# Kernel tuning notes

Hardware: AMD Instinct MI355X
Metric: run time of the kernel (lower is better)

Reference implementation:

```python
import jax, jax.numpy as jnp
import numpy as np

N = 1_000_000   # mesh points
D_IN = 5        # scalar invariants
H = 128         # hidden width
L = 5           # hidden layers
NB = 10         # tensor bases

# t0 generator basis rows (flattened 3x3 deviatoric diag tensors)
T01 = np.array([-1/3, 0, 0, 0, 1/6, 0, 0, 0, 1/6], dtype=np.float32)
T02 = np.array([1/6, 0, 0, 0, -1/3, 0, 0, 0, 1/6], dtype=np.float32)
T03 = np.array([1/6, 0, 0, 0, 1/6, 0, 0, 0, -1/3], dtype=np.float32)


def _linear_params(k, fan_in, fan_out):
    # xavier_uniform_ with gain=1.0, bias filled with 0.01 (as in init_w_and_b)
    limit = float(np.sqrt(6.0 / (fan_in + fan_out)))
    W = jax.random.uniform(k, (fan_in, fan_out), jnp.float32, -limit, limit)
    b = jnp.full((fan_out,), 0.01, jnp.float32)
    return W, b


def setup_inputs() -> dict:
    key = jax.random.key(0)
    ks = jax.random.split(key, 16)
    x = jax.random.normal(ks[0], (N, D_IN), jnp.float32)
    tb = jax.random.normal(ks[1], (N, NB, 9), jnp.float32)
    inp = {"x": x, "tb": tb}
    dims = [D_IN] + [H] * L
    for i in range(L):
        W, b = _linear_params(ks[2 + i], dims[i], dims[i + 1])
        inp[f"W{i+1}"] = W
        inp[f"b{i+1}"] = b
    inp["Wc"], inp["bc"] = _linear_params(ks[2 + L], H, NB)
    inp["Wg1"], inp["bg1"] = _linear_params(ks[3 + L], H, 1)
    inp["Wg2"], inp["bg2"] = _linear_params(ks[4 + L], H, 1)
    inp["Wg3"], inp["bg3"] = _linear_params(ks[5 + L], H, 1)
    return inp


def reference(x, tb, W1, b1, W2, b2, W3, b3, W4, b4, W5, b5,
              Wc, bc, Wg1, bg1, Wg2, bg2, Wg3, bg3):
    h = x
    for W, b in ((W1, b1), (W2, b2), (W3, b3), (W4, b4), (W5, b5)):
        h = jax.nn.relu(h @ W + b)          # [N, H]
    coeffs = h @ Wc + bc                     # [N, NB]
    g1 = h @ Wg1 + bg1                       # [N, 1]
    g2 = h @ Wg2 + bg2
    g3 = h @ Wg3 + bg3
    t0 = g1 * jnp.asarray(T01) + g2 * jnp.asarray(T02) + g3 * jnp.asarray(T03)  # [N, 9]
    # batched tensor-basis contraction replacing the per-point double loop
    bij = t0 + jnp.einsum('nt,ntc->nc', coeffs, tb)  # [N, 9]
    return bij
```

## Files before the change

kernel.cpp:

```cpp
#include <hip/hip_runtime.h>
#include <stdint.h>


#define NPTS   1000000
#define TPB    256
#define NBLKS  512
#define PTILE  128
#define NT     ((NPTS + PTILE - 1) / PTILE)

typedef uint32_t u32;
typedef __attribute__((ext_vector_type(4)))  u32   u32x4;
typedef __attribute__((ext_vector_type(8)))  short s16x8;
typedef __attribute__((ext_vector_type(16))) float f32x16;
typedef __attribute__((ext_vector_type(4), aligned(4))) float f32x4u;

#define WS_H(l)   ((l)*32768)
#define WS_Lo(l)  (131072 + (l)*32768)
#define WS_TAIL   262144
#define WS_W1     (WS_TAIL + 8192)
#define WS_BIAS   (WS_TAIL + 12288)

#define LDS_BUFH   0
#define LDS_BUFL   32768
#define LDS_HEADS  65536
#define LDS_W1     (65536 + 8192)
#define LDS_BIAS   (65536 + 12288)
#define LDS_TOTAL  81920

#define MFMA(a,b,c) __builtin_amdgcn_mfma_f32_32x32x16_bf16((a),(b),(c),0,0,0)
#define BC16(v)     __builtin_bit_cast(s16x8, (v))

__device__ __forceinline__ u32 cvtpk(float lo, float hi) {
    u32 r;
    asm("v_cvt_pk_bf16_f32 %0, %1, %2" : "=v"(r) : "v"(lo), "v"(hi));
    return r;
}
__device__ __forceinline__ float lo2f(u32 p){ return __builtin_bit_cast(float, p << 16); }
__device__ __forceinline__ float hi2f(u32 p){ return __builtin_bit_cast(float, p & 0xffff0000u); }
__device__ __forceinline__ uint16_t f2bf(float f) {
    u32 u = __builtin_bit_cast(u32, f);
    return (uint16_t)((u + 0x7fffu + ((u >> 16) & 1u)) >> 16);
}
__device__ __forceinline__ float b2f(uint16_t h){ return __builtin_bit_cast(float, (u32)h << 16); }

__device__ __forceinline__ void stage32(const char* g, char* l, int tid) {
    const int w = tid >> 6, ln = tid & 63;
    const char* gp = g + w*1024 + ln*16;
    char* lp = l + w*1024;
    #pragma unroll
    for (int i = 0; i < 8; ++i)
        __builtin_amdgcn_global_load_lds(
            (const __attribute__((address_space(1))) uint32_t*)(gp + i*4096),
            (__attribute__((address_space(3))) uint32_t*)(lp + i*4096), 16, 0, 0);
}
__device__ __forceinline__ void stage16(const char* g, char* l, int tid) {
    const int w = tid >> 6, ln = tid & 63;
    const char* gp = g + w*1024 + ln*16;
    char* lp = l + w*1024;
    #pragma unroll
    for (int i = 0; i < 4; ++i)
        __builtin_amdgcn_global_load_lds(
            (const __attribute__((address_space(1))) uint32_t*)(gp + i*4096),
            (__attribute__((address_space(3))) uint32_t*)(lp + i*4096), 16, 0, 0);
}

extern "C" __global__ void __launch_bounds__(256)
tbnn_prep(const float* __restrict__ W1, const float* __restrict__ b1,
          const float* __restrict__ W2, const float* __restrict__ b2,
          const float* __restrict__ W3, const float* __restrict__ b3,
          const float* __restrict__ W4, const float* __restrict__ b4,
          const float* __restrict__ W5, const float* __restrict__ b5,
          const float* __restrict__ Wc, const float* __restrict__ bc,
          const float* __restrict__ Wg1,const float* __restrict__ bg1,
          const float* __restrict__ Wg2,const float* __restrict__ bg2,
          const float* __restrict__ Wg3,const float* __restrict__ bg3,
          char* __restrict__ ws)
{
    int idx = blockIdx.x*256 + threadIdx.x;
    if (idx < 65536) {
        int l = idx >> 14, r = idx & 16383, ifc = r >> 7, of = r & 127;
        const float* Wt = (l==0)?W2:(l==1)?W3:(l==2)?W4:W5;
        float w = Wt[ifc*128 + of];
        uint16_t hb = f2bf(w);
        uint16_t lb = f2bf(w - b2f(hb));
        int o = (2*ifc) ^ ((of&7)<<4);
        *(uint16_t*)(ws + WS_H(l)  + of*256 + o) = hb;
        *(uint16_t*)(ws + WS_Lo(l) + of*256 + o) = lb;
    } else if (idx < 65536 + 2048) {
        int j = idx - 65536, of = j >> 7, ifc = j & 127;
        float v = 0.f;
        if      (of < 10)  v = Wc[ifc*10 + of];
        else if (of == 10) v = Wg1[ifc];
        else if (of == 11) v = Wg2[ifc];
        else if (of == 12) v = Wg3[ifc];
        uint16_t hb = f2bf(v);
        uint16_t lb = f2bf(v - b2f(hb));
        char* row = ws + WS_TAIL + of*512;
        int o = (2*ifc) ^ ((of&7)<<4);
        *(uint16_t*)(row + o)       = hb;
        *(uint16_t*)(row + 256 + o) = lb;
    } else if (idx < 65536 + 2048 + 128) {
        int of = idx - (65536 + 2048);
        uint16_t* dst = (uint16_t*)(ws + WS_W1 + of*32);
        #pragma unroll
        for (int s = 0; s < 5; ++s) {
            float w = W1[s*128 + of];
            uint16_t hb = f2bf(w);
            dst[s]      = hb;
            dst[6 + s]  = f2bf(w - b2f(hb));
            dst[11 + s] = hb;
        }
        dst[5] = f2bf(b1[of]);
    } else if (idx < 65536 + 2048 + 128 + 544) {
        int j = idx - (65536 + 2048 + 128);
        float v = 0.f;
        if (j < 512) {
            int l = j >> 7, of = j & 127;
            const float* bt = (l==0)?b2:(l==1)?b3:(l==2)?b4:b5;
            v = bt[of];
        } else {
            int of = j - 512;
            if      (of < 10)  v = bc[of];
            else if (of == 10) v = bg1[0];
            else if (of == 11) v = bg2[0];
            else if (of == 12) v = bg3[0];
        }
        *(uint16_t*)(ws + WS_BIAS + j*2) = f2bf(v);
    }
}

extern "C" __global__ void __launch_bounds__(TPB, 2)
tbnn_main(const float* __restrict__ x, const float* __restrict__ tb,
          const char* __restrict__ ws, float* __restrict__ out)
{
    extern __shared__ char smem[];
    const int tid  = threadIdx.x;
    const int wave = tid >> 6;
    const int lane = tid & 63;
    const int col  = lane & 31;
    const int hi   = lane >> 5;
    const int sm   = (col & 7) << 4;
    const int hib  = hi * 16;

    stage16(ws + WS_TAIL, smem + LDS_HEADS, tid);
    stage32(ws + WS_H(0), smem + LDS_BUFH, tid);
    __syncthreads();

    u32x4 Bc; Bc[0] = hi ? 0u : 0x00003F80u; Bc[1]=0u; Bc[2]=0u; Bc[3]=0u;
    f32x16 zf;
    #pragma unroll
    for (int i = 0; i < 16; ++i) zf[i] = 0.f;

    for (int t = blockIdx.x; t < NT; t += gridDim.x) {
        const int pb = t*PTILE + wave*32;
        const int p  = pb + col;

        f32x16 acc[4];
        u32x4  Bh[8], Bl[8];

        auto convert = [&]() {
            #pragma unroll
            for (int ot = 0; ot < 4; ++ot) {
                f32x16 a = acc[ot];
                #pragma unroll
                for (int h2 = 0; h2 < 2; ++h2) {
                    float e0 = fmaxf(a[8*h2+0], 0.f), e1 = fmaxf(a[8*h2+1], 0.f);
                    float e2 = fmaxf(a[8*h2+2], 0.f), e3 = fmaxf(a[8*h2+3], 0.f);
                    float e4 = fmaxf(a[8*h2+4], 0.f), e5 = fmaxf(a[8*h2+5], 0.f);
                    float e6 = fmaxf(a[8*h2+6], 0.f), e7 = fmaxf(a[8*h2+7], 0.f);
                    u32 h01 = cvtpk(e0,e1), h23 = cvtpk(e2,e3);
                    u32 h45 = cvtpk(e4,e5), h67 = cvtpk(e6,e7);
                    u32 l01 = cvtpk(e0 - lo2f(h01), e1 - hi2f(h01));
                    u32 l23 = cvtpk(e2 - lo2f(h23), e3 - hi2f(h23));
                    u32 l45 = cvtpk(e4 - lo2f(h45), e5 - hi2f(h45));
                    u32 l67 = cvtpk(e6 - lo2f(h67), e7 - hi2f(h67));
                    auto sh1 = __builtin_amdgcn_permlane32_swap(h01, h45, false, false);
                    auto sh2 = __builtin_amdgcn_permlane32_swap(h23, h67, false, false);
                    u32x4 fh; fh[0]=sh1[0]; fh[1]=sh2[0]; fh[2]=sh1[1]; fh[3]=sh2[1];
                    Bh[2*ot+h2] = fh;
                    auto sl1 = __builtin_amdgcn_permlane32_swap(l01, l45, false, false);
                    auto sl2 = __builtin_amdgcn_permlane32_swap(l23, l67, false, false);
                    u32x4 fl; fl[0]=sl1[0]; fl[1]=sl2[0]; fl[2]=sl1[1]; fl[3]=sl2[1];
                    Bl[2*ot+h2] = fl;
                }
            }
        };

        stage32(ws + WS_Lo(0), smem + LDS_BUFL, tid);
        {
            float x0=0.f,x1=0.f,x2=0.f,x3=0.f,x4=0.f;
            if (p < NPTS) {
                const float* xp = x + (size_t)p*5;
                f32x4u v = *(const f32x4u*)xp;
                x0=v.x; x1=v.y; x2=v.z; x3=v.w; x4=xp[4];
            }
            float h0 = lo2f(cvtpk(x0,x0)), l0 = x0 - h0;
            float h1 = lo2f(cvtpk(x1,x1)), l1 = x1 - h1;
            float h2 = lo2f(cvtpk(x2,x2)), l2 = x2 - h2;
            float h3 = lo2f(cvtpk(x3,x3)), l3 = x3 - h3;
            float h4 = lo2f(cvtpk(x4,x4)), l4 = x4 - h4;
            u32x4 Bx;
            if (hi == 0) {
                Bx[0] = cvtpk(h0,h1); Bx[1] = cvtpk(h2,h3);
                Bx[2] = cvtpk(h4,1.0f); Bx[3] = cvtpk(h0,h1);
            } else {
                Bx[0] = cvtpk(h2,h3); Bx[1] = cvtpk(h4,l0);
                Bx[2] = cvtpk(l1,l2); Bx[3] = cvtpk(l3,l4);
            }
            #pragma unroll
            for (int ot = 0; ot < 4; ++ot) {
                u32x4 Av = *(const u32x4*)(smem + LDS_W1 + (ot*32+col)*32 + hib);
                acc[ot] = MFMA(BC16(Av), BC16(Bx), zf);
            }
        }
        convert();
        __syncthreads();

        for (int l = 0; l < 4; ++l) {
            if (l) stage32(ws + WS_Lo(l), smem + LDS_BUFL, tid);
            __builtin_amdgcn_s_setprio(1);
            #pragma unroll
            for (int k = 0; k < 8; ++k) {
                int so = (k*32 + hib) ^ sm;
                const char* rp = smem + LDS_BUFH + col*256 + so;
                u32x4 A0 = *(const u32x4*)(rp);
                u32x4 A1 = *(const u32x4*)(rp + 32*256);
                u32x4 A2 = *(const u32x4*)(rp + 64*256);
                u32x4 A3 = *(const u32x4*)(rp + 96*256);
                s16x8 bl = BC16(Bl[k]), bh = BC16(Bh[k]);
                acc[0] = MFMA(BC16(A0), bl, (k==0)?zf:acc[0]);
                acc[1] = MFMA(BC16(A1), bl, (k==0)?zf:acc[1]);
                acc[2] = MFMA(BC16(A2), bl, (k==0)?zf:acc[2]);
                acc[3] = MFMA(BC16(A3), bl, (k==0)?zf:acc[3]);
                acc[0] = MFMA(BC16(A0), bh, acc[0]);
                acc[1] = MFMA(BC16(A1), bh, acc[1]);
                acc[2] = MFMA(BC16(A2), bh, acc[2]);
                acc[3] = MFMA(BC16(A3), bh, acc[3]);
            }
            __builtin_amdgcn_s_setprio(0);
            __syncthreads();

            stage32(ws + WS_H(l==3 ? 0 : l+1), smem + LDS_BUFH, tid);
            __builtin_amdgcn_s_setprio(1);
            #pragma unroll
            for (int k = 0; k < 8; ++k) {
                int so = (k*32 + hib) ^ sm;
                const char* rp = smem + LDS_BUFL + col*256 + so;
                s16x8 bh = BC16(Bh[k]);
                u32x4 A0 = *(const u32x4*)(rp);
                u32x4 A1 = *(const u32x4*)(rp + 32*256);
                u32x4 A2 = *(const u32x4*)(rp + 64*256);
                u32x4 A3 = *(const u32x4*)(rp + 96*256);
                acc[0] = MFMA(BC16(A0), bh, acc[0]);
                acc[1] = MFMA(BC16(A1), bh, acc[1]);
                acc[2] = MFMA(BC16(A2), bh, acc[2]);
                acc[3] = MFMA(BC16(A3), bh, acc[3]);
            }
            #pragma unroll
            for (int ot = 0; ot < 4; ++ot) {
                u32 bw = (u32)*(const uint16_t*)(smem + LDS_BIAS + (l*128 + ot*32 + col)*2);
                u32x4 Ab; Ab[0] = hi ? 0u : bw; Ab[1]=0u; Ab[2]=0u; Ab[3]=0u;
                acc[ot] = MFMA(BC16(Ab), BC16(Bc), acc[ot]);
            }
            __builtin_amdgcn_s_setprio(0);
            convert();
            __syncthreads();
        }

        f32x16 h6;
        __builtin_amdgcn_s_setprio(1);
        #pragma unroll
        for (int k = 0; k < 8; ++k) {
            int so = (k*32 + hib) ^ sm;
            const char* rp = smem + LDS_HEADS + (col&15)*512;
            u32x4 AvH = *(const u32x4*)(rp + so);
            u32x4 AvL = *(const u32x4*)(rp + 256 + so);
            h6 = MFMA(BC16(AvH), BC16(Bl[k]), (k==0)?zf:h6);
            h6 = MFMA(BC16(AvH), BC16(Bh[k]), h6);
            h6 = MFMA(BC16(AvL), BC16(Bh[k]), h6);
        }
        {
            u32 bw = (u32)*(const uint16_t*)(smem + LDS_BIAS + (512 + col)*2);
            u32x4 Ab; Ab[0] = hi ? 0u : bw; Ab[1]=0u; Ab[2]=0u; Ab[3]=0u;
            h6 = MFMA(BC16(Ab), BC16(Bc), h6);
        }
        __builtin_amdgcn_s_setprio(0);

        if (p < NPTS) {
            const float* tbp = tb + (size_t)p*90;
            f32x16 c = h6;
            const float sixth = 0.16666666666666666f;
            const float third = 0.3333333333333333f;
            float s[9];
            if (hi == 0) {
                float g1 = c[6], g2 = c[7];
                s[0] = -g1*third + g2*sixth;
                s[4] =  g1*sixth - g2*third;
                s[8] =  g1*sixth + g2*sixth;
            } else {
                float g3 = c[4];
                s[0] =  g3*sixth;
                s[4] =  g3*sixth;
                s[8] = -g3*third;
            }
            s[1]=s[2]=s[3]=s[5]=s[6]=s[7]=0.f;
            #pragma unroll
            for (int j = 0; j < 4; ++j) {
                int trow = (hi ? 4 : 0) + j;
                float cf = c[j];
                const float* r = tbp + trow*9;
                f32x4u r0 = *(const f32x4u*)(r);
                f32x4u r1 = *(const f32x4u*)(r + 4);
                float r8 = r[8];
                s[0] += cf*r0.x; s[1] += cf*r0.y; s[2] += cf*r0.z; s[3] += cf*r0.w;
                s[4] += cf*r1.x; s[5] += cf*r1.y; s[6] += cf*r1.z; s[7] += cf*r1.w;
                s[8] += cf*r8;
            }
            if (hi == 0) {
                #pragma unroll
                for (int j = 4; j < 6; ++j) {
                    int trow = 4 + j;
                    float cf = c[j];
                    const float* r = tbp + trow*9;
                    f32x4u r0 = *(const f32x4u*)(r);
                    f32x4u r1 = *(const f32x4u*)(r + 4);
                    float r8 = r[8];
                    s[0] += cf*r0.x; s[1] += cf*r0.y; s[2] += cf*r0.z; s[3] += cf*r0.w;
                    s[4] += cf*r1.x; s[5] += cf*r1.y; s[6] += cf*r1.z; s[7] += cf*r1.w;
                    s[8] += cf*r8;
                }
            }
            #pragma unroll
            for (int j = 0; j < 9; ++j) {
                u32 uv = __builtin_bit_cast(u32, s[j]);
                auto rr = __builtin_amdgcn_permlane32_swap(uv, uv, false, false);
                s[j] = __builtin_bit_cast(float, (u32)rr[0]) + __builtin_bit_cast(float, (u32)rr[1]);
            }
            if (hi == 0) {
                float* op = out + (size_t)p*9;
                f32x4u o0, o1;
                o0.x=s[0]; o0.y=s[1]; o0.z=s[2]; o0.w=s[3];
                o1.x=s[4]; o1.y=s[5]; o1.z=s[6]; o1.w=s[7];
                *(f32x4u*)op       = o0;
                *(f32x4u*)(op + 4) = o1;
                op[8] = s[8];
            }
        }
    }
    __syncthreads();
}

extern "C" void kernel_launch(void* const* d_in, const int* in_sizes, int n_in,
                              void* d_out, int out_size, void* d_ws, size_t ws_size,
                              hipStream_t stream) {
    (void)in_sizes; (void)n_in; (void)out_size; (void)ws_size;
    char* ws = (char*)d_ws;
    hipLaunchKernelGGL(tbnn_prep, dim3(267), dim3(256), 0, stream,
        (const float*)d_in[2],  (const float*)d_in[3],
        (const float*)d_in[4],  (const float*)d_in[5],
        (const float*)d_in[6],  (const float*)d_in[7],
        (const float*)d_in[8],  (const float*)d_in[9],
        (const float*)d_in[10], (const float*)d_in[11],
        (const float*)d_in[12], (const float*)d_in[13],
        (const float*)d_in[14], (const float*)d_in[15],
        (const float*)d_in[16], (const float*)d_in[17],
        (const float*)d_in[18], (const float*)d_in[19],
        ws);
    (void)hipFuncSetAttribute((const void*)tbnn_main,
                              hipFuncAttributeMaxDynamicSharedMemorySize, LDS_TOTAL);
    hipLaunchKernelGGL(tbnn_main, dim3(NBLKS), dim3(TPB), LDS_TOTAL, stream,
        (const float*)d_in[0], (const float*)d_in[1], ws, (float*)d_out);
}
```

Baseline: 410.3 us.

## Double-buffer interleaved hi/lo layer weights in LDS with 512-thread blocks

Packs each hidden layer's bf16 hi and lo weight halves into one interleaved 512-byte row and double-buffers whole layers in LDS (two 64KB buffers), so each layer runs in one pass and the next layer's weights stream in during compute. Blocks grow to 512 threads handling 256 points, and the swizzle widens to 16 rows. The head GEMV splits its accumulation into two chains to shorten MFMA dependency latency. The cost is 144KB of LDS per block, which allows only one block per CU and cuts latency hiding. The weight staging traffic per point also rises.

```diff
diff --git a/kernel.cpp b/kernel.cpp
--- a/kernel.cpp
+++ b/kernel.cpp
@@ -3,9 +3,9 @@
 
 
 #define NPTS   1000000
-#define TPB    256
-#define NBLKS  512
-#define PTILE  128
+#define TPB    512
+#define NBLKS  256
+#define PTILE  256
 #define NT     ((NPTS + PTILE - 1) / PTILE)
 
 typedef uint32_t u32;
@@ -14,18 +14,17 @@
 typedef __attribute__((ext_vector_type(16))) float f32x16;
 typedef __attribute__((ext_vector_type(4), aligned(4))) float f32x4u;
 
-#define WS_H(l)   ((l)*32768)
-#define WS_Lo(l)  (131072 + (l)*32768)
+#define WS_L(l)   ((l)*65536)
 #define WS_TAIL   262144
-#define WS_W1     (WS_TAIL + 8192)
-#define WS_BIAS   (WS_TAIL + 12288)
-
-#define LDS_BUFH   0
-#define LDS_BUFL   32768
-#define LDS_HEADS  65536
-#define LDS_W1     (65536 + 8192)
-#define LDS_BIAS   (65536 + 12288)
-#define LDS_TOTAL  81920
+#define WS_W1     (262144 + 8192)
+#define WS_BIAS   (262144 + 12288)
+
+#define LDS_BUF0   0
+#define LDS_BUF1   65536
+#define LDS_HEADS  131072
+#define LDS_W1     (131072 + 8192)
+#define LDS_BIAS   (131072 + 12288)
+#define LDS_TOTAL  147456
 
 #define MFMA(a,b,c) __builtin_amdgcn_mfma_f32_32x32x16_bf16((a),(b),(c),0,0,0)
 #define BC16(v)     __builtin_bit_cast(s16x8, (v))
@@ -43,25 +42,17 @@
 }
 __device__ __forceinline__ float b2f(uint16_t h){ return __builtin_bit_cast(float, (u32)h << 16); }
 
-__device__ __forceinline__ void stage32(const char* g, char* l, int tid) {
+__device__ __forceinline__ void stageN(const char* g, char* l, int tid, int nbytes) {
     const int w = tid >> 6, ln = tid & 63;
     const char* gp = g + w*1024 + ln*16;
     char* lp = l + w*1024;
     #pragma unroll
-    for (int i = 0; i < 8; ++i)
+    for (int i = 0; i < 8; ++i) {
+        if (i*8192 >= nbytes) break;
         __builtin_amdgcn_global_load_lds(
-            (const __attribute__((address_space(1))) uint32_t*)(gp + i*4096),
-            (__attribute__((address_space(3))) uint32_t*)(lp + i*4096), 16, 0, 0);
-}
-__device__ __forceinline__ void stage16(const char* g, char* l, int tid) {
-    const int w = tid >> 6, ln = tid & 63;
-    const char* gp = g + w*1024 + ln*16;
-    char* lp = l + w*1024;
-    #pragma unroll
-    for (int i = 0; i < 4; ++i)
-        __builtin_amdgcn_global_load_lds(
-            (const __attribute__((address_space(1))) uint32_t*)(gp + i*4096),
-            (__attribute__((address_space(3))) uint32_t*)(lp + i*4096), 16, 0, 0);
+            (const __attribute__((address_space(1))) uint32_t*)(gp + i*8192),
+            (__attribute__((address_space(3))) uint32_t*)(lp + i*8192), 16, 0, 0);
+    }
 }
 
 extern "C" __global__ void __launch_bounds__(256)
@@ -83,9 +74,10 @@
         float w = Wt[ifc*128 + of];
         uint16_t hb = f2bf(w);
         uint16_t lb = f2bf(w - b2f(hb));
-        int o = (2*ifc) ^ ((of&7)<<4);
-        *(uint16_t*)(ws + WS_H(l)  + of*256 + o) = hb;
-        *(uint16_t*)(ws + WS_Lo(l) + of*256 + o) = lb;
+        char* row = ws + WS_L(l) + of*512;
+        int o = (2*ifc) ^ ((of&15)<<4);
+        *(uint16_t*)(row + o)       = hb;
+        *(uint16_t*)(row + 256 + o) = lb;
     } else if (idx < 65536 + 2048) {
         int j = idx - 65536, of = j >> 7, ifc = j & 127;
         float v = 0.f;
@@ -96,7 +88,7 @@
         uint16_t hb = f2bf(v);
         uint16_t lb = f2bf(v - b2f(hb));
         char* row = ws + WS_TAIL + of*512;
-        int o = (2*ifc) ^ ((of&7)<<4);
+        int o = (2*ifc) ^ ((of&15)<<4);
         *(uint16_t*)(row + o)       = hb;
         *(uint16_t*)(row + 256 + o) = lb;
     } else if (idx < 65536 + 2048 + 128) {
@@ -129,7 +121,46 @@
     }
 }
 
-extern "C" __global__ void __launch_bounds__(TPB, 2)
+#define LAYER(lc, BUFOFF) do {                                                   \
+    const char* wb = smem + (BUFOFF);                                            \
+    __builtin_amdgcn_s_setprio(1);                                               \
+    _Pragma("unroll")                                                            \
+    for (int k = 0; k < 8; ++k) {                                                \
+        int so = (k*32 + hib) ^ sm;                                              \
+        const char* rp = wb + col*512 + so;                                      \
+        u32x4 H0 = *(const u32x4*)(rp);                                          \
+        u32x4 L0v = *(const u32x4*)(rp + 256);                                   \
+        u32x4 H1 = *(const u32x4*)(rp + 32*512);                                 \
+        u32x4 L1v = *(const u32x4*)(rp + 32*512 + 256);                          \
+        u32x4 H2 = *(const u32x4*)(rp + 64*512);                                 \
+        u32x4 L2v = *(const u32x4*)(rp + 64*512 + 256);                          \
+        u32x4 H3 = *(const u32x4*)(rp + 96*512);                                 \
+        u32x4 L3v = *(const u32x4*)(rp + 96*512 + 256);                          \
+        s16x8 bl = BC16(Bl[k]), bh = BC16(Bh[k]);                                \
+        acc[0] = MFMA(BC16(H0), bl, (k==0)?zf:acc[0]);                           \
+        acc[1] = MFMA(BC16(H1), bl, (k==0)?zf:acc[1]);                           \
+        acc[2] = MFMA(BC16(H2), bl, (k==0)?zf:acc[2]);                           \
+        acc[3] = MFMA(BC16(H3), bl, (k==0)?zf:acc[3]);                           \
+        acc[0] = MFMA(BC16(H0), bh, acc[0]);                                     \
+        acc[1] = MFMA(BC16(H1), bh, acc[1]);                                     \
+        acc[2] = MFMA(BC16(H2), bh, acc[2]);                                     \
+        acc[3] = MFMA(BC16(H3), bh, acc[3]);                                     \
+        acc[0] = MFMA(BC16(L0v), bh, acc[0]);                                    \
+        acc[1] = MFMA(BC16(L1v), bh, acc[1]);                                    \
+        acc[2] = MFMA(BC16(L2v), bh, acc[2]);                                    \
+        acc[3] = MFMA(BC16(L3v), bh, acc[3]);                                    \
+    }                                                                            \
+    _Pragma("unroll")                                                            \
+    for (int ot = 0; ot < 4; ++ot) {                                             \
+        u32 bw = (u32)*(const uint16_t*)(smem + LDS_BIAS + ((lc)*128 + ot*32 + col)*2); \
+        u32x4 Ab; Ab[0] = hi ? 0u : bw; Ab[1]=0u; Ab[2]=0u; Ab[3]=0u;            \
+        acc[ot] = MFMA(BC16(Ab), BC16(Bc), acc[ot]);                             \
+    }                                                                            \
+    __builtin_amdgcn_s_setprio(0);                                               \
+    convert();                                                                   \
+} while (0)
+
+extern "C" __global__ void __launch_bounds__(TPB)
 tbnn_main(const float* __restrict__ x, const float* __restrict__ tb,
           const char* __restrict__ ws, float* __restrict__ out)
 {
@@ -139,11 +170,12 @@
     const int lane = tid & 63;
     const int col  = lane & 31;
     const int hi   = lane >> 5;
-    const int sm   = (col & 7) << 4;
+    const int sm   = (col & 15) << 4;
     const int hib  = hi * 16;
 
-    stage16(ws + WS_TAIL, smem + LDS_HEADS, tid);
-    stage32(ws + WS_H(0), smem + LDS_BUFH, tid);
+    stageN(ws + WS_TAIL, smem + LDS_HEADS, tid, 16384);
+    stageN(ws + WS_L(0), smem + LDS_BUF0,  tid, 65536);
+    stageN(ws + WS_L(1), smem + LDS_BUF1,  tid, 65536);
     __syncthreads();
 
     u32x4 Bc; Bc[0] = hi ? 0u : 0x00003F80u; Bc[1]=0u; Bc[2]=0u; Bc[3]=0u;
@@ -186,7 +218,6 @@
             }
         };
 
-        stage32(ws + WS_Lo(0), smem + LDS_BUFL, tid);
         {
             float x0=0.f,x1=0.f,x2=0.f,x3=0.f,x4=0.f;
             if (p < NPTS) {
@@ -214,77 +245,46 @@
             }
         }
         convert();
+
+        LAYER(0, LDS_BUF0);
         __syncthreads();
-
-        for (int l = 0; l < 4; ++l) {
-            if (l) stage32(ws + WS_Lo(l), smem + LDS_BUFL, tid);
-            __builtin_amdgcn_s_setprio(1);
-            #pragma unroll
-            for (int k = 0; k < 8; ++k) {
-                int so = (k*32 + hib) ^ sm;
-                const char* rp = smem + LDS_BUFH + col*256 + so;
-                u32x4 A0 = *(const u32x4*)(rp);
-                u32x4 A1 = *(const u32x4*)(rp + 32*256);
-                u32x4 A2 = *(const u32x4*)(rp + 64*256);
-                u32x4 A3 = *(const u32x4*)(rp + 96*256);
-                s16x8 bl = BC16(Bl[k]), bh = BC16(Bh[k]);
-                acc[0] = MFMA(BC16(A0), bl, (k==0)?zf:acc[0]);
-                acc[1] = MFMA(BC16(A1), bl, (k==0)?zf:acc[1]);
-                acc[2] = MFMA(BC16(A2), bl, (k==0)?zf:acc[2]);
-                acc[3] = MFMA(BC16(A3), bl, (k==0)?zf:acc[3]);
-                acc[0] = MFMA(BC16(A0), bh, acc[0]);
-                acc[1] = MFMA(BC16(A1), bh, acc[1]);
-                acc[2] = MFMA(BC16(A2), bh, acc[2]);
-                acc[3] = MFMA(BC16(A3), bh, acc[3]);
-            }
-            __builtin_amdgcn_s_setprio(0);
-            __syncthreads();
-
-            stage32(ws + WS_H(l==3 ? 0 : l+1), smem + LDS_BUFH, tid);
-            __builtin_amdgcn_s_setprio(1);
-            #pragma unroll
-            for (int k = 0; k < 8; ++k) {
-                int so = (k*32 + hib) ^ sm;
-                const char* rp = smem + LDS_BUFL + col*256 + so;
-                s16x8 bh = BC16(Bh[k]);
-                u32x4 A0 = *(const u32x4*)(rp);
-                u32x4 A1 = *(const u32x4*)(rp + 32*256);
-                u32x4 A2 = *(const u32x4*)(rp + 64*256);
-                u32x4 A3 = *(const u32x4*)(rp + 96*256);
-                acc[0] = MFMA(BC16(A0), bh, acc[0]);
-                acc[1] = MFMA(BC16(A1), bh, acc[1]);
-                acc[2] = MFMA(BC16(A2), bh, acc[2]);
-                acc[3] = MFMA(BC16(A3), bh, acc[3]);
-            }
-            #pragma unroll
-            for (int ot = 0; ot < 4; ++ot) {
-                u32 bw = (u32)*(const uint16_t*)(smem + LDS_BIAS + (l*128 + ot*32 + col)*2);
-                u32x4 Ab; Ab[0] = hi ? 0u : bw; Ab[1]=0u; Ab[2]=0u; Ab[3]=0u;
-                acc[ot] = MFMA(BC16(Ab), BC16(Bc), acc[ot]);
-            }
-            __builtin_amdgcn_s_setprio(0);
-            convert();
-            __syncthreads();
-        }
-
-        f32x16 h6;
+        stageN(ws + WS_L(2), smem + LDS_BUF0, tid, 65536);
+        LAYER(1, LDS_BUF1);
+        __syncthreads();
+        stageN(ws + WS_L(3), smem + LDS_BUF1, tid, 65536);
+        LAYER(2, LDS_BUF0);
+        __syncthreads();
+        stageN(ws + WS_L(0), smem + LDS_BUF0, tid, 65536);
+        LAYER(3, LDS_BUF1);
+        __syncthreads();
+        stageN(ws + WS_L(1), smem + LDS_BUF1, tid, 65536);
+
+        f32x16 hA, hB;
         __builtin_amdgcn_s_setprio(1);
         #pragma unroll
         for (int k = 0; k < 8; ++k) {
             int so = (k*32 + hib) ^ sm;
             const char* rp = smem + LDS_HEADS + (col&15)*512;
-            u32x4 AvH = *(const u32x4*)(rp + so);
-            u32x4 AvL = *(const u32x4*)(rp + 256 + so);
-            h6 = MFMA(BC16(AvH), BC16(Bl[k]), (k==0)?zf:h6);
-            h6 = MFMA(BC16(AvH), BC16(Bh[k]), h6);
-            h6 = MFMA(BC16(AvL), BC16(Bh[k]), h6);
+            u32x4 HH = *(const u32x4*)(rp + so);
+            u32x4 HL = *(const u32x4*)(rp + 256 + so);
+            s16x8 bl = BC16(Bl[k]), bh = BC16(Bh[k]);
+            if (k & 1) {
+                hB = MFMA(BC16(HH), bl, (k==1)?zf:hB);
+                hB = MFMA(BC16(HH), bh, hB);
+                hB = MFMA(BC16(HL), bh, hB);
+            } else {
+                hA = MFMA(BC16(HH), bl, (k==0)?zf:hA);
+                hA = MFMA(BC16(HH), bh, hA);
+                hA = MFMA(BC16(HL), bh, hA);
+            }
         }
         {
             u32 bw = (u32)*(const uint16_t*)(smem + LDS_BIAS + (512 + col)*2);
             u32x4 Ab; Ab[0] = hi ? 0u : bw; Ab[1]=0u; Ab[2]=0u; Ab[3]=0u;
-            h6 = MFMA(BC16(Ab), BC16(Bc), h6);
+            hA = MFMA(BC16(Ab), BC16(Bc), hA);
         }
         __builtin_amdgcn_s_setprio(0);
+        f32x16 h6 = hA + hB;
 
         if (p < NPTS) {
             const float* tbp = tb + (size_t)p*90;
```

New measurement: 413.3 us. Within noise of the previous version (+0.7%).

## Prefetch tensor-basis rows early, widen LDS swizzle, split head accumulator chain

Applied to the files above, without the earlier changes.

Issues the global loads for most tensor-basis rows during the last hidden layer so their latency overlaps MFMA work instead of stalling the epilogue. It also reschedules the next layer's low-part weight staging to after the barrier, widens the LDS XOR swizzle from 8 to 16 rows to reduce bank conflicts, and splits the output-head MFMA chain into two independent accumulators to shorten the dependency chain. The prefetched registers and the unrolled layer loop raise register pressure, which could hurt occupancy at two blocks per CU.

```diff
diff --git a/kernel.cpp b/kernel.cpp
--- a/kernel.cpp
+++ b/kernel.cpp
@@ -83,7 +83,7 @@
         float w = Wt[ifc*128 + of];
         uint16_t hb = f2bf(w);
         uint16_t lb = f2bf(w - b2f(hb));
-        int o = (2*ifc) ^ ((of&7)<<4);
+        int o = (2*ifc) ^ ((of&15)<<4);
         *(uint16_t*)(ws + WS_H(l)  + of*256 + o) = hb;
         *(uint16_t*)(ws + WS_Lo(l) + of*256 + o) = lb;
     } else if (idx < 65536 + 2048) {
@@ -96,7 +96,7 @@
         uint16_t hb = f2bf(v);
         uint16_t lb = f2bf(v - b2f(hb));
         char* row = ws + WS_TAIL + of*512;
-        int o = (2*ifc) ^ ((of&7)<<4);
+        int o = (2*ifc) ^ ((of&15)<<4);
         *(uint16_t*)(row + o)       = hb;
         *(uint16_t*)(row + 256 + o) = lb;
     } else if (idx < 65536 + 2048 + 128) {
@@ -139,7 +139,7 @@
     const int lane = tid & 63;
     const int col  = lane & 31;
     const int hi   = lane >> 5;
-    const int sm   = (col & 7) << 4;
+    const int sm   = (col & 15) << 4;
     const int hib  = hi * 16;
 
     stage16(ws + WS_TAIL, smem + LDS_HEADS, tid);
@@ -151,42 +151,44 @@
     #pragma unroll
     for (int i = 0; i < 16; ++i) zf[i] = 0.f;
 
+    f32x16 acc[4];
+    u32x4  Bh[8], Bl[8];
+    f32x4u t0v[4], t1v[4];
+    float  t8v[4];
+
+    auto convert = [&]() {
+        #pragma unroll
+        for (int ot = 0; ot < 4; ++ot) {
+            f32x16 a = acc[ot];
+            #pragma unroll
+            for (int h2 = 0; h2 < 2; ++h2) {
+                float e0 = fmaxf(a[8*h2+0], 0.f), e1 = fmaxf(a[8*h2+1], 0.f);
+                float e2 = fmaxf(a[8*h2+2], 0.f), e3 = fmaxf(a[8*h2+3], 0.f);
+                float e4 = fmaxf(a[8*h2+4], 0.f), e5 = fmaxf(a[8*h2+5], 0.f);
+                float e6 = fmaxf(a[8*h2+6], 0.f), e7 = fmaxf(a[8*h2+7], 0.f);
+                u32 h01 = cvtpk(e0,e1), h23 = cvtpk(e2,e3);
+                u32 h45 = cvtpk(e4,e5), h67 = cvtpk(e6,e7);
+                u32 l01 = cvtpk(e0 - lo2f(h01), e1 - hi2f(h01));
+                u32 l23 = cvtpk(e2 - lo2f(h23), e3 - hi2f(h23));
+                u32 l45 = cvtpk(e4 - lo2f(h45), e5 - hi2f(h45));
+                u32 l67 = cvtpk(e6 - lo2f(h67), e7 - hi2f(h67));
+                auto sh1 = __builtin_amdgcn_permlane32_swap(h01, h45, false, false);
+                auto sh2 = __builtin_amdgcn_permlane32_swap(h23, h67, false, false);
+                u32x4 fh; fh[0]=sh1[0]; fh[1]=sh2[0]; fh[2]=sh1[1]; fh[3]=sh2[1];
+                Bh[2*ot+h2] = fh;
+                auto sl1 = __builtin_amdgcn_permlane32_swap(l01, l45, false, false);
+                auto sl2 = __builtin_amdgcn_permlane32_swap(l23, l67, false, false);
+                u32x4 fl; fl[0]=sl1[0]; fl[1]=sl2[0]; fl[2]=sl1[1]; fl[3]=sl2[1];
+                Bl[2*ot+h2] = fl;
+            }
+        }
+    };
+
     for (int t = blockIdx.x; t < NT; t += gridDim.x) {
-        const int pb = t*PTILE + wave*32;
-        const int p  = pb + col;
-
-        f32x16 acc[4];
-        u32x4  Bh[8], Bl[8];
-
-        auto convert = [&]() {
-            #pragma unroll
-            for (int ot = 0; ot < 4; ++ot) {
-                f32x16 a = acc[ot];
-                #pragma unroll
-                for (int h2 = 0; h2 < 2; ++h2) {
-                    float e0 = fmaxf(a[8*h2+0], 0.f), e1 = fmaxf(a[8*h2+1], 0.f);
-                    float e2 = fmaxf(a[8*h2+2], 0.f), e3 = fmaxf(a[8*h2+3], 0.f);
-                    float e4 = fmaxf(a[8*h2+4], 0.f), e5 = fmaxf(a[8*h2+5], 0.f);
-                    float e6 = fmaxf(a[8*h2+6], 0.f), e7 = fmaxf(a[8*h2+7], 0.f);
-                    u32 h01 = cvtpk(e0,e1), h23 = cvtpk(e2,e3);
-                    u32 h45 = cvtpk(e4,e5), h67 = cvtpk(e6,e7);
-                    u32 l01 = cvtpk(e0 - lo2f(h01), e1 - hi2f(h01));
-                    u32 l23 = cvtpk(e2 - lo2f(h23), e3 - hi2f(h23));
-                    u32 l45 = cvtpk(e4 - lo2f(h45), e5 - hi2f(h45));
-                    u32 l67 = cvtpk(e6 - lo2f(h67), e7 - hi2f(h67));
-                    auto sh1 = __builtin_amdgcn_permlane32_swap(h01, h45, false, false);
-                    auto sh2 = __builtin_amdgcn_permlane32_swap(h23, h67, false, false);
-                    u32x4 fh; fh[0]=sh1[0]; fh[1]=sh2[0]; fh[2]=sh1[1]; fh[3]=sh2[1];
-                    Bh[2*ot+h2] = fh;
-                    auto sl1 = __builtin_amdgcn_permlane32_swap(l01, l45, false, false);
-                    auto sl2 = __builtin_amdgcn_permlane32_swap(l23, l67, false, false);
-                    u32x4 fl; fl[0]=sl1[0]; fl[1]=sl2[0]; fl[2]=sl1[1]; fl[3]=sl2[1];
-                    Bl[2*ot+h2] = fl;
-                }
-            }
-        };
+        const int p = t*PTILE + wave*32 + col;
 
         stage32(ws + WS_Lo(0), smem + LDS_BUFL, tid);
+
         {
             float x0=0.f,x1=0.f,x2=0.f,x3=0.f,x4=0.f;
             if (p < NPTS) {
@@ -195,7 +197,7 @@
                 x0=v.x; x1=v.y; x2=v.z; x3=v.w; x4=xp[4];
             }
             float h0 = lo2f(cvtpk(x0,x0)), l0 = x0 - h0;
-            float h1 = lo2f(cvtpk(x1,x1)), l1 = x1 - h1;
+            float h1 = lo2f(cvtpk(x1,x1)), l1v = x1 - h1;
             float h2 = lo2f(cvtpk(x2,x2)), l2 = x2 - h2;
             float h3 = lo2f(cvtpk(x3,x3)), l3 = x3 - h3;
             float h4 = lo2f(cvtpk(x4,x4)), l4 = x4 - h4;
@@ -205,7 +207,7 @@
                 Bx[2] = cvtpk(h4,1.0f); Bx[3] = cvtpk(h0,h1);
             } else {
                 Bx[0] = cvtpk(h2,h3); Bx[1] = cvtpk(h4,l0);
-                Bx[2] = cvtpk(l1,l2); Bx[3] = cvtpk(l3,l4);
+                Bx[2] = cvtpk(l1v,l2); Bx[3] = cvtpk(l3,l4);
             }
             #pragma unroll
             for (int ot = 0; ot < 4; ++ot) {
@@ -216,45 +218,58 @@
         convert();
         __syncthreads();
 
+        #pragma unroll
         for (int l = 0; l < 4; ++l) {
-            if (l) stage32(ws + WS_Lo(l), smem + LDS_BUFL, tid);
             __builtin_amdgcn_s_setprio(1);
             #pragma unroll
             for (int k = 0; k < 8; ++k) {
                 int so = (k*32 + hib) ^ sm;
                 const char* rp = smem + LDS_BUFH + col*256 + so;
-                u32x4 A0 = *(const u32x4*)(rp);
-                u32x4 A1 = *(const u32x4*)(rp + 32*256);
-                u32x4 A2 = *(const u32x4*)(rp + 64*256);
-                u32x4 A3 = *(const u32x4*)(rp + 96*256);
+                u32x4 H0 = *(const u32x4*)(rp);
+                u32x4 H1 = *(const u32x4*)(rp + 8192);
+                u32x4 H2 = *(const u32x4*)(rp + 16384);
+                u32x4 H3 = *(const u32x4*)(rp + 24576);
                 s16x8 bl = BC16(Bl[k]), bh = BC16(Bh[k]);
-                acc[0] = MFMA(BC16(A0), bl, (k==0)?zf:acc[0]);
-                acc[1] = MFMA(BC16(A1), bl, (k==0)?zf:acc[1]);
-                acc[2] = MFMA(BC16(A2), bl, (k==0)?zf:acc[2]);
-                acc[3] = MFMA(BC16(A3), bl, (k==0)?zf:acc[3]);
-                acc[0] = MFMA(BC16(A0), bh, acc[0]);
-                acc[1] = MFMA(BC16(A1), bh, acc[1]);
-                acc[2] = MFMA(BC16(A2), bh, acc[2]);
-                acc[3] = MFMA(BC16(A3), bh, acc[3]);
+                acc[0] = MFMA(BC16(H0), bl, (k==0)?zf:acc[0]);
+                acc[1] = MFMA(BC16(H1), bl, (k==0)?zf:acc[1]);
+                acc[2] = MFMA(BC16(H2), bl, (k==0)?zf:acc[2]);
+                acc[3] = MFMA(BC16(H3), bl, (k==0)?zf:acc[3]);
+                acc[0] = MFMA(BC16(H0), bh, acc[0]);
+                acc[1] = MFMA(BC16(H1), bh, acc[1]);
+                acc[2] = MFMA(BC16(H2), bh, acc[2]);
+                acc[3] = MFMA(BC16(H3), bh, acc[3]);
             }
             __builtin_amdgcn_s_setprio(0);
             __syncthreads();
-
             stage32(ws + WS_H(l==3 ? 0 : l+1), smem + LDS_BUFH, tid);
+
+            if (l == 3) {
+                if (p < NPTS) {
+                    const float* tbp = tb + (size_t)p*90;
+                    #pragma unroll
+                    for (int j = 0; j < 4; ++j) {
+                        const float* r = tbp + ((hi ? 4 : 0) + j)*9;
+                        t0v[j] = *(const f32x4u*)r;
+                        t1v[j] = *(const f32x4u*)(r + 4);
+                        t8v[j] = r[8];
+                    }
+                }
+            }
+
             __builtin_amdgcn_s_setprio(1);
             #pragma unroll
             for (int k = 0; k < 8; ++k) {
                 int so = (k*32 + hib) ^ sm;
                 const char* rp = smem + LDS_BUFL + col*256 + so;
+                u32x4 L0 = *(const u32x4*)(rp);
+                u32x4 L1 = *(const u32x4*)(rp + 8192);
+                u32x4 L2 = *(const u32x4*)(rp + 16384);
+                u32x4 L3 = *(const u32x4*)(rp + 24576);
                 s16x8 bh = BC16(Bh[k]);
-                u32x4 A0 = *(const u32x4*)(rp);
-                u32x4 A1 = *(const u32x4*)(rp + 32*256);
-                u32x4 A2 = *(const u32x4*)(rp + 64*256);
-                u32x4 A3 = *(const u32x4*)(rp + 96*256);
-                acc[0] = MFMA(BC16(A0), bh, acc[0]);
-                acc[1] = MFMA(BC16(A1), bh, acc[1]);
-                acc[2] = MFMA(BC16(A2), bh, acc[2]);
-                acc[3] = MFMA(BC16(A3), bh, acc[3]);
+                acc[0] = MFMA(BC16(L0), bh, acc[0]);
+                acc[1] = MFMA(BC16(L1), bh, acc[1]);
+                acc[2] = MFMA(BC16(L2), bh, acc[2]);
+                acc[3] = MFMA(BC16(L3), bh, acc[3]);
             }
             #pragma unroll
             for (int ot = 0; ot < 4; ++ot) {
@@ -265,30 +280,38 @@
             __builtin_amdgcn_s_setprio(0);
             convert();
             __syncthreads();
-        }
-
-        f32x16 h6;
+            if (l < 3) stage32(ws + WS_Lo(l+1), smem + LDS_BUFL, tid);
+        }
+
+        f32x16 hA, hB;
         __builtin_amdgcn_s_setprio(1);
         #pragma unroll
         for (int k = 0; k < 8; ++k) {
             int so = (k*32 + hib) ^ sm;
             const char* rp = smem + LDS_HEADS + (col&15)*512;
-            u32x4 AvH = *(const u32x4*)(rp + so);
-            u32x4 AvL = *(const u32x4*)(rp + 256 + so);
-            h6 = MFMA(BC16(AvH), BC16(Bl[k]), (k==0)?zf:h6);
-            h6 = MFMA(BC16(AvH), BC16(Bh[k]), h6);
-            h6 = MFMA(BC16(AvL), BC16(Bh[k]), h6);
+            u32x4 HH = *(const u32x4*)(rp + so);
+            u32x4 HL = *(const u32x4*)(rp + 256 + so);
+            s16x8 h = BC16(HH), lo = BC16(HL);
+            if (k & 1) {
+                hB = MFMA(h,  BC16(Bl[k]), (k==1)?zf:hB);
+                hB = MFMA(h,  BC16(Bh[k]), hB);
+                hB = MFMA(lo, BC16(Bh[k]), hB);
+            } else {
+                hA = MFMA(h,  BC16(Bl[k]), (k==0)?zf:hA);
+                hA = MFMA(h,  BC16(Bh[k]), hA);
+                hA = MFMA(lo, BC16(Bh[k]), hA);
+            }
         }
         {
             u32 bw = (u32)*(const uint16_t*)(smem + LDS_BIAS + (512 + col)*2);
             u32x4 Ab; Ab[0] = hi ? 0u : bw; Ab[1]=0u; Ab[2]=0u; Ab[3]=0u;
-            h6 = MFMA(BC16(Ab), BC16(Bc), h6);
+            hA = MFMA(BC16(Ab), BC16(Bc), hA);
         }
         __builtin_amdgcn_s_setprio(0);
+        f32x16 c = hA + hB;
 
         if (p < NPTS) {
             const float* tbp = tb + (size_t)p*90;
-            f32x16 c = h6;
             const float sixth = 0.16666666666666666f;
             const float third = 0.3333333333333333f;
             float s[9];
@@ -306,12 +329,9 @@
             s[1]=s[2]=s[3]=s[5]=s[6]=s[7]=0.f;
             #pragma unroll
             for (int j = 0; j < 4; ++j) {
-                int trow = (hi ? 4 : 0) + j;
                 float cf = c[j];
-                const float* r = tbp + trow*9;
-                f32x4u r0 = *(const f32x4u*)(r);
-                f32x4u r1 = *(const f32x4u*)(r + 4);
-                float r8 = r[8];
+                f32x4u r0 = t0v[j], r1 = t1v[j];
+                float r8 = t8v[j];
                 s[0] += cf*r0.x; s[1] += cf*r0.y; s[2] += cf*r0.z; s[3] += cf*r0.w;
                 s[4] += cf*r1.x; s[5] += cf*r1.y; s[6] += cf*r1.z; s[7] += cf*r1.w;
                 s[8] += cf*r8;
@@ -319,9 +339,8 @@
             if (hi == 0) {
                 #pragma unroll
                 for (int j = 4; j < 6; ++j) {
-                    int trow = 4 + j;
                     float cf = c[j];
-                    const float* r = tbp + trow*9;
+                    const float* r = tbp + (4 + j)*9;
                     f32x4u r0 = *(const f32x4u*)(r);
                     f32x4u r1 = *(const f32x4u*)(r + 4);
                     float r8 = r[8];
```

Result: slower. 567.4 us (+38.3%).
